# Kernel tuning notes

Measured on AMD Instinct MI355X. Metric: run time of the kernel, lower is better.

## Reference

```python
import jax, jax.numpy as jnp
import numpy as np


def setup_inputs() -> dict:
    key = jax.random.key(0)
    k1, k2 = jax.random.split(key)
    B, H, W, C = 8, 384, 1280, 8
    U = jax.random.normal(k1, (B, H, W, C), dtype=jnp.float32)
    flo = jax.random.normal(k2, (B, H, W, 2), dtype=jnp.float32)
    return {"U": U, "flo": flo}


def _forward_warp(U, flo):
    # Faithful port of transformerFwd: bilinear forward splatting.
    B, H, W, C = U.shape
    out_h, out_w = H, W  # out_size == (H, W) as used in get_occlusion_mask_from_flow
    # normalized sampling grid in [-1, 1]
    x_s = jnp.linspace(-1.0, 1.0, out_w, dtype=jnp.float32)  # [W]
    y_s = jnp.linspace(-1.0, 1.0, out_h, dtype=jnp.float32)  # [H]
    x_t = x_s[None, None, :] + flo[..., 0] / ((out_w - 1.0) / 2.0)  # [B,H,W]
    y_t = y_s[None, :, None] + flo[..., 1] / ((out_h - 1.0) / 2.0)  # [B,H,W]
    # map back to pixel coords
    x = (x_t.reshape(-1) + 1.0) * (W - 1.0) / 2.0  # [B*H*W]
    y = (y_t.reshape(-1) + 1.0) * (H - 1.0) / 2.0
    x0 = jnp.floor(x).astype(jnp.int32)
    x1 = x0 + 1
    y0 = jnp.floor(y).astype(jnp.int32)
    y1 = y0 + 1
    x0c = jnp.clip(x0, 0, W - 1)
    x1c = jnp.clip(x1, 0, W - 1)
    y0c = jnp.clip(y0, 0, H - 1)
    y1c = jnp.clip(y1, 0, H - 1)
    # flat destination indices into [B*H*W]
    base = jnp.repeat(jnp.arange(B, dtype=jnp.int32) * (H * W), out_h * out_w)
    idx_a = base + y0c * W + x0c
    idx_b = base + y1c * W + x0c
    idx_c = base + y0c * W + x1c
    idx_d = base + y1c * W + x1c
    x0f = x0.astype(jnp.float32)
    x1f = x1.astype(jnp.float32)
    y0f = y0.astype(jnp.float32)
    y1f = y1.astype(jnp.float32)
    # bilinear weights, zeroed where the tap fell out of bounds (clamp changed it)
    wa = jnp.where((x0c == x0) & (y0c == y0), (x1f - x) * (y1f - y), 0.0)
    wb = jnp.where((x0c == x0) & (y1c == y1), (x1f - x) * (y - y0f), 0.0)
    wc = jnp.where((x1c == x1) & (y0c == y0), (x - x0f) * (y1f - y), 0.0)
    wd = jnp.where((x1c == x1) & (y1c == y1), (x - x0f) * (y - y0f), 0.0)
    im_flat = U.reshape(-1, C)  # [B*H*W, C]
    out = jnp.zeros((B * H * W, C), dtype=jnp.float32)
    out = out.at[idx_a].add(im_flat * wa[:, None])
    out = out.at[idx_b].add(im_flat * wb[:, None])
    out = out.at[idx_c].add(im_flat * wc[:, None])
    out = out.at[idx_d].add(im_flat * wd[:, None])
    return out.reshape(B, out_h, out_w, C)


def reference(U, flo):
    return _forward_warp(U, flo)
```

## Files before the change

kernel.cpp:

```cpp
#include <hip/hip_runtime.h>
#include <math.h>

constexpr int Bc = 8, Hc = 384, Wc = 1280, Cc = 8;

constexpr int TH = 16, TW = 16;
constexpr int WIN = 3;
constexpr float FMAX = 3.0f;
constexpr int RH = TH + 2 * WIN;
constexpr int RW = TW + 2 * WIN;
constexpr int PSTR = RW + 1;
constexpr int TILES_X = Wc / TW;
constexpr int TILES_Y = Hc / TH;
constexpr int BLK = 256;
constexpr unsigned LIST_CAP = 262144;
constexpr size_t WS_NEED = 16 + (size_t)LIST_CAP * 4;

__global__ __launch_bounds__(BLK) void fwd_warp_gather(
    const float* __restrict__ U, const float* __restrict__ flo,
    float* __restrict__ out, unsigned* __restrict__ ws, int do_append)
{
    __shared__ float2 sxy[RH * PSTR];

    int tile = blockIdx.x;
    int b  = tile / (TILES_X * TILES_Y);
    int r  = tile % (TILES_X * TILES_Y);
    int Y0 = (r / TILES_X) * TH;
    int X0 = (r % TILES_X) * TW;
    int t  = threadIdx.x;

    const float2* flo2 = reinterpret_cast<const float2*>(flo);
    const float4* u4   = reinterpret_cast<const float4*>(U);

    for (int i = t; i < RH * RW; i += BLK) {
        int sy = i / RW, sx = i - sy * RW;
        int h = Y0 - WIN + sy;
        int w = X0 - WIN + sx;
        bool inimg = ((unsigned)h < (unsigned)Hc) & ((unsigned)w < (unsigned)Wc);
        int hc = min(max(h, 0), Hc - 1);
        int wc = min(max(w, 0), Wc - 1);
        int sidx = (b * Hc + hc) * Wc + wc;
        float2 f = flo2[sidx];
        bool inl = (fabsf(f.x) <= FMAX) && (fabsf(f.y) <= FMAX);
        float2 v = (inimg && inl) ? make_float2((float)w + f.x, (float)h + f.y)
                                  : make_float2(-1e9f, -1e9f);
        sxy[sy * PSTR + sx] = v;
        if (do_append && inimg && !inl &&
            sy >= WIN && sy < WIN + TH && sx >= WIN && sx < WIN + TW) {
            unsigned pos = atomicAdd(ws, 1u);
            if (pos < LIST_CAP) ws[4 + pos] = (unsigned)sidx;
        }
    }
    __syncthreads();

    int lpy = t >> 4, lpx = t & 15;
    int py = Y0 + lpy, px = X0 + lpx;
    float pxf = (float)px, pyf = (float)py;
    int pixbase = (b * Hc + py) * Wc + px;

    unsigned long long mask = 0ull;
    #pragma unroll
    for (int dy = 0; dy < 2 * WIN + 1; ++dy) {
        int rb = (lpy + dy) * PSTR + lpx;
        #pragma unroll
        for (int dx = 0; dx < 2 * WIN + 1; ++dx) {
            float2 s = sxy[rb + dx];
            float m = fmaxf(fabsf(s.x - pxf), fabsf(s.y - pyf));
            unsigned long long hit = (m < 1.0f) ? 1ull : 0ull;
            mask |= hit << (dy * 8 + dx);
        }
    }

    float a0 = 0.f, a1 = 0.f, a2 = 0.f, a3 = 0.f;
    float a4 = 0.f, a5 = 0.f, a6 = 0.f, a7 = 0.f;
    while (mask) {
        int bit = __builtin_ctzll(mask);
        mask &= mask - 1;
        int dy = bit >> 3, dx = bit & 7;
        float2 s = sxy[(lpy + dy) * PSTR + lpx + dx];
        float wgt = (1.0f - fabsf(s.x - pxf)) * (1.0f - fabsf(s.y - pyf));
        int sidx = pixbase + (dy - WIN) * Wc + (dx - WIN);
        float4 ua = u4[(size_t)sidx * 2];
        float4 ub = u4[(size_t)sidx * 2 + 1];
        a0 += ua.x * wgt; a1 += ua.y * wgt;
        a2 += ua.z * wgt; a3 += ua.w * wgt;
        a4 += ub.x * wgt; a5 += ub.y * wgt;
        a6 += ub.z * wgt; a7 += ub.w * wgt;
    }

    float4 o0 = {a0, a1, a2, a3};
    float4 o1 = {a4, a5, a6, a7};
    reinterpret_cast<float4*>(out)[(size_t)pixbase * 2]     = o0;
    reinterpret_cast<float4*>(out)[(size_t)pixbase * 2 + 1] = o1;
}

__global__ __launch_bounds__(BLK) void fwd_warp_outlier_list(
    const float* __restrict__ U, const float* __restrict__ flo,
    float* __restrict__ out, const unsigned* __restrict__ ws)
{
    unsigned n = min(ws[0], LIST_CAP);
    for (unsigned i = blockIdx.x * BLK + threadIdx.x; i < n;
         i += gridDim.x * BLK) {
        int sidx = (int)ws[4 + i];
        int w = sidx % Wc;
        int h = (sidx / Wc) % Hc;
        float2 f = reinterpret_cast<const float2*>(flo)[sidx];

        float x = (float)w + f.x;
        float y = (float)h + f.y;
        float x0f = floorf(x), y0f = floorf(y);
        int x0 = (int)x0f, y0 = (int)y0f;
        float wx[2] = { (x0f + 1.0f) - x, x - x0f };
        float wy[2] = { (y0f + 1.0f) - y, y - y0f };

        const float4* u4 = reinterpret_cast<const float4*>(U);
        float4 ua = u4[(size_t)sidx * 2];
        float4 ub = u4[(size_t)sidx * 2 + 1];
        int bbase = sidx - (h * Wc + w);

        #pragma unroll
        for (int j = 0; j < 2; ++j) {
            #pragma unroll
            for (int k = 0; k < 2; ++k) {
                int ty = y0 + j, tx = x0 + k;
                if ((unsigned)ty < (unsigned)Hc && (unsigned)tx < (unsigned)Wc) {
                    float wgt = wx[k] * wy[j];
                    if (wgt != 0.0f) {
                        float* p = out + ((size_t)(bbase + ty * Wc + tx)) * 8;
                        atomicAdd(p + 0, ua.x * wgt);
                        atomicAdd(p + 1, ua.y * wgt);
                        atomicAdd(p + 2, ua.z * wgt);
                        atomicAdd(p + 3, ua.w * wgt);
                        atomicAdd(p + 4, ub.x * wgt);
                        atomicAdd(p + 5, ub.y * wgt);
                        atomicAdd(p + 6, ub.z * wgt);
                        atomicAdd(p + 7, ub.w * wgt);
                    }
                }
            }
        }
    }
}

__global__ __launch_bounds__(BLK) void fwd_warp_outlier_scan(
    const float* __restrict__ U, const float* __restrict__ flo,
    float* __restrict__ out)
{
    int tid = blockIdx.x * BLK + threadIdx.x;
    int total = Bc * Hc * Wc;
    if (tid >= total) return;
    float2 f = reinterpret_cast<const float2*>(flo)[tid];
    if (fabsf(f.x) <= FMAX && fabsf(f.y) <= FMAX) return;

    int w = tid % Wc;
    int h = (tid / Wc) % Hc;
    float x = (float)w + f.x;
    float y = (float)h + f.y;
    float x0f = floorf(x), y0f = floorf(y);
    int x0 = (int)x0f, y0 = (int)y0f;
    float wx[2] = { (x0f + 1.0f) - x, x - x0f };
    float wy[2] = { (y0f + 1.0f) - y, y - y0f };

    const float4* u4 = reinterpret_cast<const float4*>(U);
    float4 ua = u4[(size_t)tid * 2];
    float4 ub = u4[(size_t)tid * 2 + 1];
    int bbase = tid - (h * Wc + w);

    #pragma unroll
    for (int j = 0; j < 2; ++j) {
        #pragma unroll
        for (int k = 0; k < 2; ++k) {
            int ty = y0 + j, tx = x0 + k;
            if ((unsigned)ty < (unsigned)Hc && (unsigned)tx < (unsigned)Wc) {
                float wgt = wx[k] * wy[j];
                if (wgt != 0.0f) {
                    float* p = out + ((size_t)(bbase + ty * Wc + tx)) * 8;
                    atomicAdd(p + 0, ua.x * wgt);
                    atomicAdd(p + 1, ua.y * wgt);
                    atomicAdd(p + 2, ua.z * wgt);
                    atomicAdd(p + 3, ua.w * wgt);
                    atomicAdd(p + 4, ub.x * wgt);
                    atomicAdd(p + 5, ub.y * wgt);
                    atomicAdd(p + 6, ub.z * wgt);
                    atomicAdd(p + 7, ub.w * wgt);
                }
            }
        }
    }
}

extern "C" void kernel_launch(void* const* d_in, const int* in_sizes, int n_in,
                              void* d_out, int out_size, void* d_ws, size_t ws_size,
                              hipStream_t stream)
{
    const float* U   = (const float*)d_in[0];
    const float* flo = (const float*)d_in[1];
    float* out = (float*)d_out;
    unsigned* ws = (unsigned*)d_ws;

    bool use_list = (ws != nullptr) && (ws_size >= WS_NEED);
    int grid_g = Bc * TILES_X * TILES_Y;

    if (use_list) {
        hipMemsetAsync(d_ws, 0, 16, stream);
        fwd_warp_gather<<<grid_g, BLK, 0, stream>>>(U, flo, out, ws, 1);
        fwd_warp_outlier_list<<<256, BLK, 0, stream>>>(U, flo, out, ws);
    } else {
        fwd_warp_gather<<<grid_g, BLK, 0, stream>>>(U, flo, out, ws, 0);
        int grid_o = (Bc * Hc * Wc + BLK - 1) / BLK;
        fwd_warp_outlier_scan<<<grid_o, BLK, 0, stream>>>(U, flo, out);
    }
}
```

Baseline: 443.6 us.

## Compute a 2x2 output quad per thread with software-prefetched gathers

```diff
diff --git a/kernel.cpp b/kernel.cpp
--- a/kernel.cpp
+++ b/kernel.cpp
@@ -3,7 +3,7 @@
 
 constexpr int Bc = 8, Hc = 384, Wc = 1280, Cc = 8;
 
-constexpr int TH = 16, TW = 16;
+constexpr int TH = 32, TW = 32;
 constexpr int WIN = 3;
 constexpr float FMAX = 3.0f;
 constexpr int RH = TH + 2 * WIN;
@@ -14,6 +14,12 @@
 constexpr int BLK = 256;
 constexpr unsigned LIST_CAP = 262144;
 constexpr size_t WS_NEED = 16 + (size_t)LIST_CAP * 4;
+
+__device__ __forceinline__ void fma4(float4& a, float4 u, float w)
+{
+    a.x = fmaf(u.x, w, a.x); a.y = fmaf(u.y, w, a.y);
+    a.z = fmaf(u.z, w, a.z); a.w = fmaf(u.w, w, a.w);
+}
 
 __global__ __launch_bounds__(BLK) void fwd_warp_gather(
     const float* __restrict__ U, const float* __restrict__ flo,
@@ -52,45 +58,74 @@
     }
     __syncthreads();
 
-    int lpy = t >> 4, lpx = t & 15;
+    int qy = t >> 4, qx = t & 15;
+    int lpy = qy * 2, lpx = qx * 2;
     int py = Y0 + lpy, px = X0 + lpx;
-    float pxf = (float)px, pyf = (float)py;
-    int pixbase = (b * Hc + py) * Wc + px;
+    float cx = (float)px + 0.5f;
+    float cy = (float)py + 0.5f;
 
     unsigned long long mask = 0ull;
     #pragma unroll
-    for (int dy = 0; dy < 2 * WIN + 1; ++dy) {
+    for (int dy = 0; dy < 8; ++dy) {
         int rb = (lpy + dy) * PSTR + lpx;
         #pragma unroll
-        for (int dx = 0; dx < 2 * WIN + 1; ++dx) {
+        for (int dx = 0; dx < 8; ++dx) {
             float2 s = sxy[rb + dx];
-            float m = fmaxf(fabsf(s.x - pxf), fabsf(s.y - pyf));
-            unsigned long long hit = (m < 1.0f) ? 1ull : 0ull;
+            float m = fmaxf(fabsf(s.x - cx), fabsf(s.y - cy));
+            unsigned long long hit = (m < 1.5f) ? 1ull : 0ull;
             mask |= hit << (dy * 8 + dx);
         }
     }
 
-    float a0 = 0.f, a1 = 0.f, a2 = 0.f, a3 = 0.f;
-    float a4 = 0.f, a5 = 0.f, a6 = 0.f, a7 = 0.f;
-    while (mask) {
-        int bit = __builtin_ctzll(mask);
-        mask &= mask - 1;
+    float4 aA0 = {0,0,0,0}, aB0 = {0,0,0,0};
+    float4 aA1 = {0,0,0,0}, aB1 = {0,0,0,0};
+    float4 aA2 = {0,0,0,0}, aB2 = {0,0,0,0};
+    float4 aA3 = {0,0,0,0}, aB3 = {0,0,0,0};
+
+    int sbase = (b * Hc + Y0 - WIN) * Wc + (X0 - WIN);
+    float pxf = (float)px, pyf = (float)py;
+
+    float2 s; float4 ua, ub;
+    bool have = (mask != 0ull);
+    if (have) {
+        int bit = __builtin_ctzll(mask); mask &= mask - 1;
         int dy = bit >> 3, dx = bit & 7;
-        float2 s = sxy[(lpy + dy) * PSTR + lpx + dx];
-        float wgt = (1.0f - fabsf(s.x - pxf)) * (1.0f - fabsf(s.y - pyf));
-        int sidx = pixbase + (dy - WIN) * Wc + (dx - WIN);
-        float4 ua = u4[(size_t)sidx * 2];
-        float4 ub = u4[(size_t)sidx * 2 + 1];
-        a0 += ua.x * wgt; a1 += ua.y * wgt;
-        a2 += ua.z * wgt; a3 += ua.w * wgt;
-        a4 += ub.x * wgt; a5 += ub.y * wgt;
-        a6 += ub.z * wgt; a7 += ub.w * wgt;
-    }
-
-    float4 o0 = {a0, a1, a2, a3};
-    float4 o1 = {a4, a5, a6, a7};
-    reinterpret_cast<float4*>(out)[(size_t)pixbase * 2]     = o0;
-    reinterpret_cast<float4*>(out)[(size_t)pixbase * 2 + 1] = o1;
+        s = sxy[(lpy + dy) * PSTR + lpx + dx];
+        int sidx = sbase + (lpy + dy) * Wc + (lpx + dx);
+        ua = u4[(size_t)sidx * 2];
+        ub = u4[(size_t)sidx * 2 + 1];
+    }
+    while (have) {
+        float2 sn; float4 uan, ubn;
+        bool haven = (mask != 0ull);
+        if (haven) {
+            int bit = __builtin_ctzll(mask); mask &= mask - 1;
+            int dy = bit >> 3, dx = bit & 7;
+            sn = sxy[(lpy + dy) * PSTR + lpx + dx];
+            int sidx = sbase + (lpy + dy) * Wc + (lpx + dx);
+            uan = u4[(size_t)sidx * 2];
+            ubn = u4[(size_t)sidx * 2 + 1];
+        }
+        float tx = s.x - pxf, ty = s.y - pyf;
+        float bx0 = fmaxf(0.f, 1.f - fabsf(tx));
+        float bx1 = fmaxf(0.f, 1.f - fabsf(tx - 1.f));
+        float by0 = fmaxf(0.f, 1.f - fabsf(ty));
+        float by1 = fmaxf(0.f, 1.f - fabsf(ty - 1.f));
+        float w00 = bx0 * by0, w01 = bx1 * by0;
+        float w10 = bx0 * by1, w11 = bx1 * by1;
+        fma4(aA0, ua, w00); fma4(aB0, ub, w00);
+        fma4(aA1, ua, w01); fma4(aB1, ub, w01);
+        fma4(aA2, ua, w10); fma4(aB2, ub, w10);
+        fma4(aA3, ua, w11); fma4(aB3, ub, w11);
+        s = sn; ua = uan; ub = ubn; have = haven;
+    }
+
+    float4* o4 = reinterpret_cast<float4*>(out);
+    size_t obase = (size_t)(b * Hc + py) * Wc + px;
+    o4[obase * 2]            = aA0; o4[obase * 2 + 1]            = aB0;
+    o4[(obase + 1) * 2]      = aA1; o4[(obase + 1) * 2 + 1]      = aB1;
+    o4[(obase + Wc) * 2]     = aA2; o4[(obase + Wc) * 2 + 1]     = aB2;
+    o4[(obase + Wc + 1) * 2] = aA3; o4[(obase + Wc + 1) * 2 + 1] = aB3;
 }
 
 __global__ __launch_bounds__(BLK) void fwd_warp_outlier_list(
```

Result: slower. 478.7 us (+7.9%).
